# Optimization experiments

Measured on AMD Instinct MI355X. Metric: run time of the kernel, lower is better.

The kernel has to match this reference:

```python
import jax, jax.numpy as jnp
import numpy as np

B, N, C, H = 4096, 49, 128, 4
DH = C // H  # head dim = 32
SCALE = DH ** -0.5

def setup_inputs() -> dict:
    key = jax.random.key(0)
    kx, kq, kp, kb = jax.random.split(key, 4)
    x = jax.random.normal(kx, (B, N, C), dtype=jnp.float32)
    w_qkv = jax.random.normal(kq, (C, 3 * C), dtype=jnp.float32) * (C ** -0.5)
    w_proj = jax.random.normal(kp, (C, C), dtype=jnp.float32) * (C ** -0.5)
    b_proj = jax.random.normal(kb, (C,), dtype=jnp.float32) * 0.01
    return {"x": x, "w_qkv": w_qkv, "w_proj": w_proj, "b_proj": b_proj}

def reference(x, w_qkv, w_proj, b_proj):
    Bx, Nx, Cx = x.shape
    qkv = x @ w_qkv  # (B, N, 3C)
    q, k, v = jnp.split(qkv, 3, axis=-1)
    # (B, N, C) -> (B, H, N, DH)
    def heads(t):
        return t.reshape(Bx, Nx, H, DH).transpose(0, 2, 1, 3)
    q, k, v = heads(q), heads(k), heads(v)
    attn = jnp.einsum('bhnd,bhmd->bhnm', q, k) * SCALE
    attn = jax.nn.softmax(attn, axis=-1)
    out = jnp.einsum('bhnm,bhmd->bhnd', attn, v)
    out = out.transpose(0, 2, 1, 3).reshape(Bx, Nx, Cx)
    return out @ w_proj + b_proj
```

## Files before the change

kernel.cpp:

```cpp
#include <hip/hip_runtime.h>
#include <hip/hip_bf16.h>

typedef unsigned short u16;
typedef __bf16 bf16;
typedef __attribute__((ext_vector_type(8))) __bf16 bf16x8;
typedef __attribute__((ext_vector_type(4))) __bf16 bf16x4;
typedef __attribute__((ext_vector_type(4))) float f32x4;

#define MFMA16(A,B,C) __builtin_amdgcn_mfma_f32_16x16x32_bf16(A,B,C,0,0,0)

constexpr int NTOK = 49;
constexpr int CH   = 128;
constexpr float CEXP = 0.17677669529663687f * 1.4426950408889634f;

__device__ __forceinline__ bf16x8 lds_v8(const char* p) {
    return *reinterpret_cast<const bf16x8*>(p);
}
__device__ __forceinline__ void lds_st64(char* p, float a0, float a1, float a2, float a3) {
    bf16x4 v = {(bf16)a0, (bf16)a1, (bf16)a2, (bf16)a3};
    *reinterpret_cast<bf16x4*>(p) = v;
}

__global__ void prep_weights_kernel(const float* __restrict__ wqkv,
                                    const float* __restrict__ wproj,
                                    bf16* __restrict__ ws) {
    int i = blockIdx.x * 256 + threadIdx.x;
    if (i < 384 * 128) {
        int n = i >> 7, k = i & 127;
        ws[i] = (bf16)wqkv[k * 384 + n];
    }
    if (i < 128 * 128) {
        int n = i >> 7, k = i & 127;
        ws[384 * 128 + i] = (bf16)wproj[k * 128 + n];
    }
}

__launch_bounds__(256, 3)
__global__ void fused_window_attn(const float* __restrict__ x,
                                  const bf16* __restrict__ wqkv_t,
                                  const bf16* __restrict__ wproj_t,
                                  const float* __restrict__ bias,
                                  float* __restrict__ out) {
    __shared__ __align__(16) u16 smem[24576];
    char* S8 = reinterpret_cast<char*>(smem);

    const int tid  = threadIdx.x;
    const int blk  = blockIdx.x;
    const int h    = tid >> 6;
    const int lane = tid & 63;
    const int lr   = lane & 15;
    const int lg   = lane >> 4;

    char* Qb = S8 + h * 4096;
    char* Kb = S8 + 16384 + h * 4096;
    char* Vb = S8 + 32768 + h * 4096;

    const float* xw = x + (size_t)blk * (NTOK * CH);
    #pragma unroll
    for (int it = 0; it < 7; ++it) {
        int i = tid + it * 256;
        if (i < (NTOK * CH) / 4) {
            float4 v = reinterpret_cast<const float4*>(xw)[i];
            int e = i * 4, row = e >> 7, col = e & 127;
            bf16x4 pk4 = { (bf16)v.x, (bf16)v.y, (bf16)v.z, (bf16)v.w };
            *reinterpret_cast<bf16x4*>(S8 + row * 256 + ((col * 2) ^ ((row & 7) << 4))) = pk4;
        }
    }
    if (tid < 240) {
        uint4 zz = {0, 0, 0, 0};
        *reinterpret_cast<uint4*>(S8 + 49 * 256 + tid * 16) = zz;
    }
    __syncthreads();

    bf16x8 xf[4][4];
    #pragma unroll
    for (int tt = 0; tt < 4; ++tt)
        #pragma unroll
        for (int ks = 0; ks < 4; ++ks) {
            int row = tt * 16 + lr;
            xf[tt][ks] = lds_v8(S8 + row * 256 + ((ks * 64 + lg * 16) ^ ((row & 7) << 4)));
        }
    __syncthreads();

    __builtin_amdgcn_s_setprio(1);
    #pragma unroll
    for (int mt = 0; mt < 4; ++mt) {
        int ct = (mt < 2) ? (2 * h + mt) : (8 + 2 * h + (mt - 2));
        bf16x8 wf[4];
        const bf16* wrow = wqkv_t + (ct * 16 + lr) * 128 + lg * 8;
        #pragma unroll
        for (int ks = 0; ks < 4; ++ks)
            wf[ks] = *reinterpret_cast<const bf16x8*>(wrow + ks * 32);
        char* dst = (mt < 2) ? Qb : Kb;
        int dh0 = (mt & 1) * 16 + lg * 4;
        #pragma unroll
        for (int tt = 0; tt < 4; ++tt) {
            f32x4 a = {0.f, 0.f, 0.f, 0.f};
            #pragma unroll
            for (int ks = 0; ks < 4; ++ks) a = MFMA16(wf[ks], xf[tt][ks], a);
            int tok = tt * 16 + lr;
            lds_st64(dst + tok * 64 + ((dh0 * 2) ^ ((tok & 7) << 3)),
                     a[0], a[1], a[2], a[3]);
        }
    }
    #pragma unroll
    for (int i = 0; i < 2; ++i) {
        int ct = 16 + 2 * h + i;
        bf16x8 wf[4];
        const bf16* wrow = wqkv_t + (ct * 16 + lr) * 128 + lg * 8;
        #pragma unroll
        for (int ks = 0; ks < 4; ++ks)
            wf[ks] = *reinterpret_cast<const bf16x8*>(wrow + ks * 32);
        int dh = i * 16 + lr;
        #pragma unroll
        for (int tt = 0; tt < 4; ++tt) {
            f32x4 a = {0.f, 0.f, 0.f, 0.f};
            #pragma unroll
            for (int ks = 0; ks < 4; ++ks) a = MFMA16(xf[tt][ks], wf[ks], a);
            lds_st64(Vb + dh * 128 + ((tt * 32 + lg * 8) ^ ((dh & 7) << 4)),
                     a[0], a[1], a[2], a[3]);
        }
    }
    __builtin_amdgcn_s_setprio(0);

    bf16x8 qf[4], kf[4];
    #pragma unroll
    for (int t = 0; t < 4; ++t) {
        int row = t * 16 + lr;
        int o0 = row * 64 + ((lg * 16) ^ ((row & 7) << 3));
        bf16x4 qlo = *reinterpret_cast<const bf16x4*>(Qb + o0);
        bf16x4 qhi = *reinterpret_cast<const bf16x4*>(Qb + (o0 ^ 8));
        bf16x4 klo = *reinterpret_cast<const bf16x4*>(Kb + o0);
        bf16x4 khi = *reinterpret_cast<const bf16x4*>(Kb + (o0 ^ 8));
        bf16x8 q8 = { qlo[0],qlo[1],qlo[2],qlo[3], qhi[0],qhi[1],qhi[2],qhi[3] };
        bf16x8 k8 = { klo[0],klo[1],klo[2],klo[3], khi[0],khi[1],khi[2],khi[3] };
        qf[t] = q8;
        kf[t] = k8;
    }
    bf16x8 vf[2][2];
    #pragma unroll
    for (int dht = 0; dht < 2; ++dht)
        #pragma unroll
        for (int ks2 = 0; ks2 < 2; ++ks2) {
            int dh = dht * 16 + lr;
            vf[dht][ks2] = lds_v8(Vb + dh * 128 + ((ks2 * 64 + lg * 16) ^ ((dh & 7) << 4)));
        }

    float rs[4];
    #pragma unroll
    for (int qt = 0; qt < 4; ++qt) {
        f32x4 s[4];
        __builtin_amdgcn_s_setprio(1);
        #pragma unroll
        for (int st = 0; st < 4; ++st) {
            f32x4 z = {0.f, 0.f, 0.f, 0.f};
            s[st] = MFMA16(kf[st], qf[qt], z);
        }
        __builtin_amdgcn_s_setprio(0);
        float l = 0.f;
        #pragma unroll
        for (int st = 0; st < 3; ++st)
            #pragma unroll
            for (int rg = 0; rg < 4; ++rg) {
                float e = exp2f(s[st][rg] * CEXP);
                s[st][rg] = e;
                l += e;
            }
        {
            float e48 = exp2f(s[3][0] * CEXP);
            float v48 = (lg == 0) ? e48 : 0.f;
            s[3][0] = v48; s[3][1] = 0.f; s[3][2] = 0.f; s[3][3] = 0.f;
            l += v48;
        }
        l += __shfl_xor(l, 16);
        l += __shfl_xor(l, 32);
        rs[qt] = 1.f / l;
        int q = qt * 16 + lr;
        char* pb = (qt < 2) ? (Qb + q * 128) : (Kb + (q - 32) * 128);
        #pragma unroll
        for (int st = 0; st < 4; ++st)
            lds_st64(pb + ((st * 32 + lg * 8) ^ ((q & 7) << 4)),
                     s[st][0], s[st][1], s[st][2], s[st][3]);
    }

    f32x4 o[2][4];
    #pragma unroll
    for (int dht = 0; dht < 2; ++dht)
        #pragma unroll
        for (int qt = 0; qt < 4; ++qt) { f32x4 z = {0.f,0.f,0.f,0.f}; o[dht][qt] = z; }
    __builtin_amdgcn_s_setprio(1);
    #pragma unroll
    for (int ks2 = 0; ks2 < 2; ++ks2)
        #pragma unroll
        for (int qt = 0; qt < 4; ++qt) {
            int q = qt * 16 + lr;
            const char* pb = (qt < 2) ? (Qb + q * 128) : (Kb + (q - 32) * 128);
            bf16x8 pf = lds_v8(pb + ((ks2 * 64 + lg * 16) ^ ((q & 7) << 4)));
            o[0][qt] = MFMA16(vf[0][ks2], pf, o[0][qt]);
            o[1][qt] = MFMA16(vf[1][ks2], pf, o[1][qt]);
        }
    __builtin_amdgcn_s_setprio(0);
    __syncthreads();

    #pragma unroll
    for (int qt = 0; qt < 4; ++qt) {
        int q = qt * 16 + lr;
        float scl = rs[qt];
        #pragma unroll
        for (int dht = 0; dht < 2; ++dht)
            lds_st64(S8 + q * 256 + ((h * 64 + dht * 32 + lg * 8) ^ ((q & 7) << 4)),
                     o[dht][qt][0] * scl, o[dht][qt][1] * scl,
                     o[dht][qt][2] * scl, o[dht][qt][3] * scl);
    }
    __syncthreads();

    bf16x8 ofr[4][4];
    #pragma unroll
    for (int tt = 0; tt < 4; ++tt)
        #pragma unroll
        for (int ks = 0; ks < 4; ++ks) {
            int row = tt * 16 + lr;
            ofr[tt][ks] = lds_v8(S8 + row * 256 + ((ks * 64 + lg * 16) ^ ((row & 7) << 4)));
        }
    #pragma unroll
    for (int i = 0; i < 2; ++i) {
        int ct = 2 * h + i;
        bf16x8 wf[4];
        const bf16* wrow = wproj_t + (ct * 16 + lr) * 128 + lg * 8;
        #pragma unroll
        for (int ks = 0; ks < 4; ++ks)
            wf[ks] = *reinterpret_cast<const bf16x8*>(wrow + ks * 32);
        float4 bv = *reinterpret_cast<const float4*>(bias + ct * 16 + lg * 4);
        __builtin_amdgcn_s_setprio(1);
        #pragma unroll
        for (int tt = 0; tt < 4; ++tt) {
            f32x4 a = {0.f, 0.f, 0.f, 0.f};
            #pragma unroll
            for (int ks = 0; ks < 4; ++ks) a = MFMA16(wf[ks], ofr[tt][ks], a);
            int tok = tt * 16 + lr;
            if (tok < NTOK) {
                float4 r = { a[0] + bv.x, a[1] + bv.y, a[2] + bv.z, a[3] + bv.w };
                *reinterpret_cast<float4*>(
                    out + ((size_t)blk * NTOK + tok) * CH + ct * 16 + lg * 4) = r;
            }
        }
        __builtin_amdgcn_s_setprio(0);
    }
}

extern "C" void kernel_launch(void* const* d_in, const int* in_sizes, int n_in,
                              void* d_out, int out_size, void* d_ws, size_t ws_size,
                              hipStream_t stream) {
    const float* x     = (const float*)d_in[0];
    const float* wqkv  = (const float*)d_in[1];
    const float* wproj = (const float*)d_in[2];
    const float* bias  = (const float*)d_in[3];
    float* out = (float*)d_out;
    bf16* ws   = (bf16*)d_ws;

    constexpr size_t WS_NEED = (size_t)(384 * 128 + 128 * 128) * sizeof(u16);
    if (ws_size < WS_NEED) return;

    prep_weights_kernel<<<192, 256, 0, stream>>>(wqkv, wproj, ws);
    fused_window_attn<<<4096, 256, 0, stream>>>(x, ws, ws + 384 * 128, bias, out);
}
```

Baseline: 97.13 us.

## Keep Q, K and softmax probabilities in registers via lane shuffles instead of LDS

Q and K projection results and the softmax probability tiles are now packed to bf16 and redistributed into MFMA operand layout with cross-lane shuffles, no longer round-tripping through shared memory. This removes the Q/K LDS buffers, shrinking shared memory from 48KB to 32KB, and the launch bound is raised to allow 4 blocks per CU. The PV product is fused into the per-query-tile softmax loop, and one barrier is dropped. In exchange it issues many ds_bpermute shuffles and adds register pressure, which may spill under the tighter occupancy bound.

After: 91.82 us. 5.5% less time.

```diff
diff --git a/kernel.cpp b/kernel.cpp
--- a/kernel.cpp
+++ b/kernel.cpp
@@ -2,6 +2,7 @@
 #include <hip/hip_bf16.h>
 
 typedef unsigned short u16;
+typedef unsigned int u32;
 typedef __bf16 bf16;
 typedef __attribute__((ext_vector_type(8))) __bf16 bf16x8;
 typedef __attribute__((ext_vector_type(4))) __bf16 bf16x4;
@@ -19,6 +20,21 @@
 __device__ __forceinline__ void lds_st64(char* p, float a0, float a1, float a2, float a3) {
     bf16x4 v = {(bf16)a0, (bf16)a1, (bf16)a2, (bf16)a3};
     *reinterpret_cast<bf16x4*>(p) = v;
+}
+__device__ __forceinline__ u32 pkbf(float a, float b) {
+    u16 lo = __builtin_bit_cast(u16, (bf16)a);
+    u16 hi = __builtin_bit_cast(u16, (bf16)b);
+    return (u32)lo | ((u32)hi << 16);
+}
+
+__device__ __forceinline__ bf16x8 xchg(u32 lo0, u32 lo1, u32 hi0, u32 hi1,
+                                       int srcA, int srcB, bool hiT) {
+    u32 a0 = __shfl(lo0, srcA), b0 = __shfl(hi0, srcA);
+    u32 a1 = __shfl(lo1, srcA), b1 = __shfl(hi1, srcA);
+    u32 a2 = __shfl(lo0, srcB), b2 = __shfl(hi0, srcB);
+    u32 a3 = __shfl(lo1, srcB), b3 = __shfl(hi1, srcB);
+    uint4 u = { hiT ? b0 : a0, hiT ? b1 : a1, hiT ? b2 : a2, hiT ? b3 : a3 };
+    return __builtin_bit_cast(bf16x8, u);
 }
 
 __global__ void prep_weights_kernel(const float* __restrict__ wqkv,
@@ -35,13 +51,13 @@
     }
 }
 
-__launch_bounds__(256, 3)
+__launch_bounds__(256, 4)
 __global__ void fused_window_attn(const float* __restrict__ x,
                                   const bf16* __restrict__ wqkv_t,
                                   const bf16* __restrict__ wproj_t,
                                   const float* __restrict__ bias,
                                   float* __restrict__ out) {
-    __shared__ __align__(16) u16 smem[24576];
+    __shared__ __align__(16) u16 smem[16384];
     char* S8 = reinterpret_cast<char*>(smem);
 
     const int tid  = threadIdx.x;
@@ -50,10 +66,11 @@
     const int lane = tid & 63;
     const int lr   = lane & 15;
     const int lg   = lane >> 4;
-
-    char* Qb = S8 + h * 4096;
-    char* Kb = S8 + 16384 + h * 4096;
-    char* Vb = S8 + 32768 + h * 4096;
+    const int srcA = lr + 32 * (lg & 1);
+    const int srcB = srcA + 16;
+    const bool hiT = (lg >= 2);
+
+    char* Vb = S8 + 16384 + h * 4096;
 
     const float* xw = x + (size_t)blk * (NTOK * CH);
     #pragma unroll
@@ -80,29 +97,8 @@
             int row = tt * 16 + lr;
             xf[tt][ks] = lds_v8(S8 + row * 256 + ((ks * 64 + lg * 16) ^ ((row & 7) << 4)));
         }
-    __syncthreads();
 
     __builtin_amdgcn_s_setprio(1);
-    #pragma unroll
-    for (int mt = 0; mt < 4; ++mt) {
-        int ct = (mt < 2) ? (2 * h + mt) : (8 + 2 * h + (mt - 2));
-        bf16x8 wf[4];
-        const bf16* wrow = wqkv_t + (ct * 16 + lr) * 128 + lg * 8;
-        #pragma unroll
-        for (int ks = 0; ks < 4; ++ks)
-            wf[ks] = *reinterpret_cast<const bf16x8*>(wrow + ks * 32);
-        char* dst = (mt < 2) ? Qb : Kb;
-        int dh0 = (mt & 1) * 16 + lg * 4;
-        #pragma unroll
-        for (int tt = 0; tt < 4; ++tt) {
-            f32x4 a = {0.f, 0.f, 0.f, 0.f};
-            #pragma unroll
-            for (int ks = 0; ks < 4; ++ks) a = MFMA16(wf[ks], xf[tt][ks], a);
-            int tok = tt * 16 + lr;
-            lds_st64(dst + tok * 64 + ((dh0 * 2) ^ ((tok & 7) << 3)),
-                     a[0], a[1], a[2], a[3]);
-        }
-    }
     #pragma unroll
     for (int i = 0; i < 2; ++i) {
         int ct = 16 + 2 * h + i;
@@ -121,22 +117,59 @@
                      a[0], a[1], a[2], a[3]);
         }
     }
+
+    bf16x8 qf[4];
+    {
+        u32 pkq[2][4][2];
+        #pragma unroll
+        for (int half = 0; half < 2; ++half) {
+            int ct = 2 * h + half;
+            bf16x8 wf[4];
+            const bf16* wrow = wqkv_t + (ct * 16 + lr) * 128 + lg * 8;
+            #pragma unroll
+            for (int ks = 0; ks < 4; ++ks)
+                wf[ks] = *reinterpret_cast<const bf16x8*>(wrow + ks * 32);
+            #pragma unroll
+            for (int tt = 0; tt < 4; ++tt) {
+                f32x4 a = {0.f, 0.f, 0.f, 0.f};
+                #pragma unroll
+                for (int ks = 0; ks < 4; ++ks) a = MFMA16(wf[ks], xf[tt][ks], a);
+                pkq[half][tt][0] = pkbf(a[0], a[1]);
+                pkq[half][tt][1] = pkbf(a[2], a[3]);
+            }
+        }
+        #pragma unroll
+        for (int tt = 0; tt < 4; ++tt)
+            qf[tt] = xchg(pkq[0][tt][0], pkq[0][tt][1],
+                          pkq[1][tt][0], pkq[1][tt][1], srcA, srcB, hiT);
+    }
+    bf16x8 kf[4];
+    {
+        u32 pkk[2][4][2];
+        #pragma unroll
+        for (int half = 0; half < 2; ++half) {
+            int ct = 8 + 2 * h + half;
+            bf16x8 wf[4];
+            const bf16* wrow = wqkv_t + (ct * 16 + lr) * 128 + lg * 8;
+            #pragma unroll
+            for (int ks = 0; ks < 4; ++ks)
+                wf[ks] = *reinterpret_cast<const bf16x8*>(wrow + ks * 32);
+            #pragma unroll
+            for (int tt = 0; tt < 4; ++tt) {
+                f32x4 a = {0.f, 0.f, 0.f, 0.f};
+                #pragma unroll
+                for (int ks = 0; ks < 4; ++ks) a = MFMA16(wf[ks], xf[tt][ks], a);
+                pkk[half][tt][0] = pkbf(a[0], a[1]);
+                pkk[half][tt][1] = pkbf(a[2], a[3]);
+            }
+        }
+        #pragma unroll
+        for (int tt = 0; tt < 4; ++tt)
+            kf[tt] = xchg(pkk[0][tt][0], pkk[0][tt][1],
+                          pkk[1][tt][0], pkk[1][tt][1], srcA, srcB, hiT);
+    }
     __builtin_amdgcn_s_setprio(0);
 
-    bf16x8 qf[4], kf[4];
-    #pragma unroll
-    for (int t = 0; t < 4; ++t) {
-        int row = t * 16 + lr;
-        int o0 = row * 64 + ((lg * 16) ^ ((row & 7) << 3));
-        bf16x4 qlo = *reinterpret_cast<const bf16x4*>(Qb + o0);
-        bf16x4 qhi = *reinterpret_cast<const bf16x4*>(Qb + (o0 ^ 8));
-        bf16x4 klo = *reinterpret_cast<const bf16x4*>(Kb + o0);
-        bf16x4 khi = *reinterpret_cast<const bf16x4*>(Kb + (o0 ^ 8));
-        bf16x8 q8 = { qlo[0],qlo[1],qlo[2],qlo[3], qhi[0],qhi[1],qhi[2],qhi[3] };
-        bf16x8 k8 = { klo[0],klo[1],klo[2],klo[3], khi[0],khi[1],khi[2],khi[3] };
-        qf[t] = q8;
-        kf[t] = k8;
-    }
     bf16x8 vf[2][2];
     #pragma unroll
     for (int dht = 0; dht < 2; ++dht)
@@ -145,8 +178,8 @@
             int dh = dht * 16 + lr;
             vf[dht][ks2] = lds_v8(Vb + dh * 128 + ((ks2 * 64 + lg * 16) ^ ((dh & 7) << 4)));
         }
-
-    float rs[4];
+    __syncthreads();
+
     #pragma unroll
     for (int qt = 0; qt < 4; ++qt) {
         f32x4 s[4];
@@ -174,43 +207,30 @@
         }
         l += __shfl_xor(l, 16);
         l += __shfl_xor(l, 32);
-        rs[qt] = 1.f / l;
+        float rs = 1.f / l;
+
+        u32 pks[4][2];
+        #pragma unroll
+        for (int st = 0; st < 4; ++st) {
+            pks[st][0] = pkbf(s[st][0], s[st][1]);
+            pks[st][1] = pkbf(s[st][2], s[st][3]);
+        }
+        bf16x8 pf0 = xchg(pks[0][0], pks[0][1], pks[1][0], pks[1][1], srcA, srcB, hiT);
+        bf16x8 pf1 = xchg(pks[2][0], pks[2][1], pks[3][0], pks[3][1], srcA, srcB, hiT);
+
+        f32x4 o0 = {0.f, 0.f, 0.f, 0.f}, o1 = {0.f, 0.f, 0.f, 0.f};
+        __builtin_amdgcn_s_setprio(1);
+        o0 = MFMA16(vf[0][0], pf0, o0);
+        o1 = MFMA16(vf[1][0], pf0, o1);
+        o0 = MFMA16(vf[0][1], pf1, o0);
+        o1 = MFMA16(vf[1][1], pf1, o1);
+        __builtin_amdgcn_s_setprio(0);
+
         int q = qt * 16 + lr;
-        char* pb = (qt < 2) ? (Qb + q * 128) : (Kb + (q - 32) * 128);
-        #pragma unroll
-        for (int st = 0; st < 4; ++st)
-            lds_st64(pb + ((st * 32 + lg * 8) ^ ((q & 7) << 4)),
-                     s[st][0], s[st][1], s[st][2], s[st][3]);
-    }
-
-    f32x4 o[2][4];
-    #pragma unroll
-    for (int dht = 0; dht < 2; ++dht)
-        #pragma unroll
-        for (int qt = 0; qt < 4; ++qt) { f32x4 z = {0.f,0.f,0.f,0.f}; o[dht][qt] = z; }
-    __builtin_amdgcn_s_setprio(1);
-    #pragma unroll
-    for (int ks2 = 0; ks2 < 2; ++ks2)
-        #pragma unroll
-        for (int qt = 0; qt < 4; ++qt) {
-            int q = qt * 16 + lr;
-            const char* pb = (qt < 2) ? (Qb + q * 128) : (Kb + (q - 32) * 128);
-            bf16x8 pf = lds_v8(pb + ((ks2 * 64 + lg * 16) ^ ((q & 7) << 4)));
-            o[0][qt] = MFMA16(vf[0][ks2], pf, o[0][qt]);
-            o[1][qt] = MFMA16(vf[1][ks2], pf, o[1][qt]);
-        }
-    __builtin_amdgcn_s_setprio(0);
-    __syncthreads();
-
-    #pragma unroll
-    for (int qt = 0; qt < 4; ++qt) {
-        int q = qt * 16 + lr;
-        float scl = rs[qt];
-        #pragma unroll
-        for (int dht = 0; dht < 2; ++dht)
-            lds_st64(S8 + q * 256 + ((h * 64 + dht * 32 + lg * 8) ^ ((q & 7) << 4)),
-                     o[dht][qt][0] * scl, o[dht][qt][1] * scl,
-                     o[dht][qt][2] * scl, o[dht][qt][3] * scl);
+        lds_st64(S8 + q * 256 + ((h * 64 + lg * 8) ^ ((q & 7) << 4)),
+                 o0[0] * rs, o0[1] * rs, o0[2] * rs, o0[3] * rs);
+        lds_st64(S8 + q * 256 + ((h * 64 + 32 + lg * 8) ^ ((q & 7) << 4)),
+                 o1[0] * rs, o1[1] * rs, o1[2] * rs, o1[3] * rs);
     }
     __syncthreads();
 
```
